# Performance work log

Hardware: AMD Instinct MI355X
Metric: run time of the kernel (lower is better)

The kernel has to match this reference:

```python
import jax, jax.numpy as jnp
import numpy as np
import math

# ----- sizes -----
NUM_EDGES = 16384
NUM_NODES = 1024          # senders index into [0, NUM_NODES)
N_MUL = 64                # multiplicity n = V.shape[1]
AVG_NEIGH = 16.0          # avg_num_neighbors
F_IN = 64                 # scalar feature dim of x

# ----- real spherical harmonics (component normalization: sum_m Y_lm^2 = 2l+1) -----
_S3 = math.sqrt(3.0); _S5 = math.sqrt(5.0); _S15 = math.sqrt(15.0)
_C33 = math.sqrt(70.0)/4.0; _C32 = math.sqrt(105.0)/2.0
_C31 = math.sqrt(42.0)/4.0; _C30 = math.sqrt(7.0)/2.0; _CXYZ = math.sqrt(105.0)

def _sph(vn):
    x, y, z = vn[:, 0], vn[:, 1], vn[:, 2]
    Y0 = jnp.ones_like(x)[:, None]
    Y1 = _S3 * vn
    Y2 = jnp.stack([_S15*x*y, _S15*y*z, 0.5*_S5*(3*z*z - 1), _S15*x*z, 0.5*_S15*(x*x - y*y)], axis=1)
    Y3 = jnp.stack([_C33*y*(3*x*x - y*y), _CXYZ*x*y*z, _C31*y*(5*z*z - 1), _C30*z*(5*z*z - 3), _C31*x*(5*z*z - 1), _C32*z*(x*x - y*y), _C33*x*(x*x - 3*y*y)], axis=1)
    return [Y0, Y1, Y2, Y3]

# monomial form of the same SH, used to derive EXACT Clebsch-Gordan coefficients
_SHP = {
    0: [[(1.0, (0,0,0))]],
    1: [[(_S3, (1,0,0))], [(_S3, (0,1,0))], [(_S3, (0,0,1))]],
    2: [[(_S15, (1,1,0))], [(_S15, (0,1,1))], [(1.5*_S5, (0,0,2)), (-0.5*_S5, (0,0,0))], [(_S15, (1,0,1))], [(0.5*_S15, (2,0,0)), (-0.5*_S15, (0,2,0))]],
    3: [[(3*_C33, (2,1,0)), (-_C33, (0,3,0))], [(_CXYZ, (1,1,1))], [(5*_C31, (0,1,2)), (-_C31, (0,1,0))], [(5*_C30, (0,0,3)), (-3*_C30, (0,0,1))], [(5*_C31, (1,0,2)), (-_C31, (1,0,0))], [(_C32, (2,0,1)), (-_C32, (0,2,1))], [(_C33, (3,0,0)), (-3*_C33, (1,2,0))]],
}

def _dfact(n):
    r = 1
    while n > 1:
        r *= n; n -= 2
    return r

def _mono_int(e):
    # exact integral of x^a y^b z^c over the unit sphere
    a, b, c = e
    if (a % 2) or (b % 2) or (c % 2):
        return 0.0
    return 4.0*math.pi*_dfact(a-1)*_dfact(b-1)*_dfact(c-1)/_dfact(a+b+c+1)

def _pmul(p, q):
    return [(cp*cq, (a1+a2, b1+b2, c1+c2)) for cp, (a1,b1,c1) in p for cq, (a2,b2,c2) in q]

def _pint(p):
    return sum(c*_mono_int(e) for c, e in p)

def _cg(l1, l2, l3):
    # unique SO(3) intertwiner in this real-SH basis, scaled like e3nn component norm: sqrt(2l3+1)*w3j
    C = np.zeros((2*l1+1, 2*l2+1, 2*l3+1))
    for i, p1 in enumerate(_SHP[l1]):
        for j, p2 in enumerate(_SHP[l2]):
            p12 = _pmul(p1, p2)
            for k, p3 in enumerate(_SHP[l3]):
                C[i, j, k] = _pint(_pmul(p12, p3)) / (4.0*math.pi)
    return jnp.asarray(C / np.linalg.norm(C) * np.sqrt(2*l3+1), dtype=jnp.float32)

# tensor-product paths surviving filter_ir_out = 0e + 1o + 2e (inputs: SH 0e+1o+2e+3o, V 0e+1o+2e)
_PATHS0 = [(0,0), (1,1), (2,2)]
_PATHS1 = [(0,1), (1,0), (1,2), (2,1), (3,2)]
_PATHS2 = [(0,2), (1,1), (2,0), (2,2), (3,1)]
CGS = {(l1, l2, l3): _cg(l1, l2, l3) for l3, ps in ((0, _PATHS0), (1, _PATHS1), (2, _PATHS2)) for l1, l2 in ps}

# e3nn normalize_function(silu): divide by sqrt(E_{z~N(0,1)}[silu(z)^2])
_zg = np.linspace(-12.0, 12.0, 200001)
_phi = np.exp(-0.5*_zg*_zg)/np.sqrt(2.0*np.pi)
_sl = _zg/(1.0 + np.exp(-_zg))
ACT_C = float(np.sqrt(np.sum(_sl*_sl*_phi)*(_zg[1]-_zg[0])))

def _nsilu(v):
    return jax.nn.silu(v) / ACT_C

def _forward(vectors, x, V, senders, W_w, W1, W2, W3, Wv1, Wv2):
    E, n = V.shape[0], V.shape[1]
    d = jnp.linalg.norm(vectors, axis=1, keepdims=True)                 # [E,1] edge lengths
    vn = vectors / d
    Y = jnp.concatenate(_sph(vn), axis=1)                               # [E,16], ell = 0..3
    w = (x @ W_w) / math.sqrt(x.shape[1])                               # [E,n] edge weights (1-layer MLP, no act)
    wY = w[:, :, None] * Y[:, None, :]                                  # [E,n,16]
    agg = jax.ops.segment_sum(wY, senders, num_segments=NUM_NODES)[senders]  # scatter_sum + map_back
    agg = agg / math.sqrt(AVG_NEIGH)
    A = jnp.split(agg, [1, 4, 9], axis=2)                               # SH chunks: dims 1,3,5,7
    B = jnp.split(V, [1, 4], axis=2)                                    # V chunks: dims 1,3,5
    def tp(l1, l2, l3):
        return jnp.einsum('eni,enj,ijk->enk', A[l1], B[l2], CGS[(l1, l2, l3)])
    scal = jnp.concatenate([tp(a, b, 0) for a, b in _PATHS0], axis=2)   # [E,n,3] new scalars
    V1 = jnp.concatenate([tp(a, b, 1) for a, b in _PATHS1], axis=1)     # [E,5n,3] 1o paths
    V2 = jnp.concatenate([tp(a, b, 2) for a, b in _PATHS2], axis=1)     # [E,5n,5] 2e paths
    h = jnp.concatenate([x, scal.reshape(E, 3*n)], axis=1)              # [E, F_IN+3n]
    h = _nsilu(h @ W1 / math.sqrt(h.shape[1]))
    h = _nsilu(h @ W2 / math.sqrt(W2.shape[0]))
    h = h @ W3 / math.sqrt(W3.shape[0])                                 # output_activation=False
    # poly_envelope(p-1=5, 2), p=6: 1 - 28 d^6 + 48 d^7 - 21 d^8 on [0,1), 0 outside
    u = 1.0 - 28.0*d**6 + 48.0*d**7 - 21.0*d**8
    x_out = jnp.where(d < 1.0, u, 0.0) * h                              # [E,64]
    o1 = jnp.einsum('emi,mo->eoi', V1, Wv1) / math.sqrt(V1.shape[1])    # Linear per irrep: [E,n,3]
    o2 = jnp.einsum('emi,mo->eoi', V2, Wv2) / math.sqrt(V2.shape[1])    # [E,n,5]
    # output 0e block has no input path -> zeros (e3nn Linear, no bias)
    V_out = jnp.concatenate([jnp.zeros((E, n, 1), x_out.dtype), o1, o2], axis=2)  # [E,n,9]
    return x_out, V_out

def setup_inputs():
    key = jax.random.key(0)
    ks = jax.random.split(key, 10)
    E = NUM_EDGES
    vectors = 0.35 * jax.random.normal(ks[0], (E, 3), jnp.float32)   # mostly inside cutoff radius 1
    x = jax.random.normal(ks[1], (E, F_IN), jnp.float32)
    V = jax.random.normal(ks[2], (E, N_MUL, 9), jnp.float32)
    senders = jax.random.randint(ks[3], (E,), 0, NUM_NODES, dtype=jnp.int32)
    W_w = jax.random.normal(ks[4], (F_IN, N_MUL), jnp.float32)
    W1 = jax.random.normal(ks[5], (F_IN + 3*N_MUL, 64), jnp.float32)
    W2 = jax.random.normal(ks[6], (64, 64), jnp.float32)
    W3 = jax.random.normal(ks[7], (64, 64), jnp.float32)
    Wv1 = jax.random.normal(ks[8], (5*N_MUL, N_MUL), jnp.float32)
    Wv2 = jax.random.normal(ks[9], (5*N_MUL, N_MUL), jnp.float32)
    return {"vectors": vectors, "x": x, "V": V, "senders": senders, "W_w": W_w, "W1": W1, "W2": W2, "W3": W3, "Wv1": Wv1, "Wv2": Wv2}

def reference(vectors, x, V, senders, W_w, W1, W2, W3, Wv1, Wv2):
    return _forward(vectors, x, V, senders, W_w, W1, W2, W3, Wv1, Wv2)
```

## Files before the change

### kernel.cpp

```cpp
#include <hip/hip_runtime.h>
#include <math.h>

#define NNODES 1024
#define EB 4

typedef __attribute__((ext_vector_type(8))) short short8;
typedef __attribute__((ext_vector_type(4))) float f32x4;

__device__ __forceinline__ unsigned short f2bf(float f) {
  union { float f; unsigned int u; } v; v.f = f;
  unsigned int r = v.u + 0x7fffu + ((v.u >> 16) & 1u);
  return (unsigned short)(r >> 16);
}

__device__ __constant__ int PL1[13] = {0,1,2, 0,1,1,2,3, 0,1,2,2,3};
__device__ __constant__ int PL2[13] = {0,1,2, 1,0,2,1,2, 2,1,0,2,1};
__device__ __constant__ int PL3[13] = {0,0,0, 1,1,1,1,1, 2,2,2,2,2};
__device__ __constant__ int PCG[13] = {0,1,10, 35,44,53,98,143, 248,273,318,343,468};

__device__ __constant__ double SHC[16][2] = {
  {1.0, 0.0},
  {1.7320508075688772, 0.0},
  {1.7320508075688772, 0.0},
  {1.7320508075688772, 0.0},
  {3.8729833462074170, 0.0},
  {3.8729833462074170, 0.0},
  {3.3541019662496844, -1.1180339887498949},
  {3.8729833462074170, 0.0},
  {1.9364916731037085, -1.9364916731037085},
  {6.2749501990055667, -2.0916500663351889},
  {10.246950765959598, 0.0},
  {8.1009258730098255, -1.6201851746019651},
  {6.6143782776614768, -3.9686269665968861},
  {8.1009258730098255, -1.6201851746019651},
  {5.1234753829797990, -5.1234753829797990},
  {2.0916500663351889, -6.2749501990055667},
};
__device__ __constant__ int SHE[16][2] = {
  {0,0},{1,0},{16,0},{256,0},
  {17,0},{272,0},{512,0},{257,0},{2,32},
  {18,48},{273,0},{528,16},{768,256},{513,1},{258,288},{3,33}};

__global__ __launch_bounds__(256) void k_const(
    float* __restrict__ cg, float* __restrict__ actp, int* __restrict__ counts)
{
  const int bid = blockIdx.x;
  const int t = threadIdx.x;

  if (bid < 13) {
    if (bid < 4) counts[bid*256 + t] = 0;
    __shared__ double sh[256];
    const int p = bid;
    const int LOFF[4] = {0,1,4,9};
    int l1 = PL1[p], l2 = PL2[p], l3 = PL3[p];
    int n1 = 2*l1+1, n2 = 2*l2+1, n3 = 2*l3+1;
    int nent = n1*n2*n3;
    const unsigned long long DP =
        1ULL | (1ULL<<7) | (1ULL<<14) | (2ULL<<21) | (3ULL<<28)
      | (8ULL<<35) | (15ULL<<42) | (48ULL<<49) | (105ULL<<56);
    double v = 0.0;
    if (t < nent) {
      int i = t / (n2*n3);
      int rem = t - i*(n2*n3);
      int j = rem / n3;
      int k = rem - j*n3;
      int lm1 = LOFF[l1]+i, lm2 = LOFF[l2]+j, lm3 = LOFF[l3]+k;
      double cs1[2] = {SHC[lm1][0], SHC[lm1][1]}; int es1[2] = {SHE[lm1][0], SHE[lm1][1]};
      double cs2[2] = {SHC[lm2][0], SHC[lm2][1]}; int es2[2] = {SHE[lm2][0], SHE[lm2][1]};
      double cs3[2] = {SHC[lm3][0], SHC[lm3][1]}; int es3[2] = {SHE[lm3][0], SHE[lm3][1]};
      #pragma unroll
      for (int t1 = 0; t1 < 2; t1++)
      #pragma unroll
      for (int t2 = 0; t2 < 2; t2++)
      #pragma unroll
      for (int t3 = 0; t3 < 2; t3++) {
        double cc = cs1[t1]*cs2[t2]*cs3[t3];
        int s = es1[t1] + es2[t2] + es3[t3];
        int a = s & 15, b = (s >> 4) & 15, c = (s >> 8) & 15;
        if (!((a|b|c) & 1)) {
          double num = (double)(int)((DP >> (7*a)) & 127)
                     * (double)(int)((DP >> (7*b)) & 127)
                     * (double)(int)((DP >> (7*c)) & 127);
          double den = (double)(int)((DP >> (7*(a+b+c+2))) & 127);
          v += cc * (num / den);
        }
      }
    }
    sh[t] = (t < nent) ? v*v : 0.0;
    __syncthreads();
    for (int d = 128; d > 0; d >>= 1) {
      if (t < d) sh[t] += sh[t+d];
      __syncthreads();
    }
    double scale = sqrt((double)(2*l3+1)) / sqrt(sh[0]);
    if (t < nent) cg[PCG[p] + t] = (float)(v * scale * 0.25);

  } else {
    __shared__ float shf[256];
    const int b = bid - 13;
    const float dz = 24.0f / 200000.0f;
    float s = 0.f;
    for (int i = b*256 + t; i <= 200000; i += 8*256) {
      float z = -12.0f + dz * (float)i;
      float ph = __expf(-0.5f * z * z) * 0.3989422804014327f;
      float sl = z / (1.f + __expf(-z));
      s = fmaf(sl*sl, ph, s);
    }
    shf[t] = s;
    __syncthreads();
    for (int d = 128; d > 0; d >>= 1) {
      if (t < d) shf[t] += shf[t + d];
      __syncthreads();
    }
    if (t == 0) actp[b] = shf[0];
  }
}

__global__ __launch_bounds__(256) void k_pre(
    const int* __restrict__ senders, int* __restrict__ counts, int* __restrict__ elist,
    const float* __restrict__ Wv1, const float* __restrict__ Wv2,
    const float* __restrict__ W1, const float* __restrict__ W2, const float* __restrict__ W3,
    unsigned short* __restrict__ wv1f, unsigned short* __restrict__ wv2f,
    unsigned short* __restrict__ w1f, unsigned short* __restrict__ w2f,
    unsigned short* __restrict__ w3f,
    const float* __restrict__ actp, int E)
{
  const int t = threadIdx.x;
  const int nsc = gridDim.x - 32;
  if ((int)blockIdx.x < nsc) {
    int e = blockIdx.x*256 + t;
    if (e < E) {
      int s = senders[e];
      int pos = atomicAdd(&counts[s], 1) & 63;
      elist[s*64 + pos] = e;
    }
    return;
  }
  const int wid = t >> 6, lane = t & 63;
  const int g = (blockIdx.x - nsc)*4 + wid;
  const float ia = rsqrtf((actp[0]+actp[1]+actp[2]+actp[3]
                          +actp[4]+actp[5]+actp[6]+actp[7]) * (24.0f/200000.0f));
  const float s320 = 0.05590169943749474f;
  const float* src; unsigned short* dst; int nk, f; float sc;
  if (g < 40)       { src = Wv1; dst = wv1f; nk = 10; f = g;       sc = s320; }
  else if (g < 80)  { src = Wv2; dst = wv2f; nk = 10; f = g - 40;  sc = s320; }
  else if (g < 112) { src = W1;  dst = w1f;  nk = 8;  f = g - 80;  sc = 0.0625f; }
  else if (g < 120) { src = W2;  dst = w2f;  nk = 2;  f = g - 112; sc = 0.125f*ia; }
  else              { src = W3;  dst = w3f;  nk = 2;  f = g - 120; sc = 0.125f*ia; }
  int nt = f / nk;
  int ks = f - nt*nk;
  unsigned short us[8];
  #pragma unroll
  for (int j = 0; j < 8; j++) {
    float v = src[(ks*32 + (lane>>4)*8 + j)*64 + nt*16 + (lane & 15)];
    us[j] = f2bf(v * sc);
  }
  uint4 pk;
  pk.x = (unsigned)us[0] | ((unsigned)us[1] << 16);
  pk.y = (unsigned)us[2] | ((unsigned)us[3] << 16);
  pk.z = (unsigned)us[4] | ((unsigned)us[5] << 16);
  pk.w = (unsigned)us[6] | ((unsigned)us[7] << 16);
  *(uint4*)(dst + ((size_t)f*64 + lane)*8) = pk;
}

__global__ __launch_bounds__(256) void k_node(
    const float* __restrict__ vec, const float* __restrict__ x,
    const float* __restrict__ Ww,
    const int* __restrict__ counts, const int* __restrict__ elist,
    float* __restrict__ node_agg)
{
  __shared__ float red[4*1024];
  const int wid = threadIdx.x >> 6, lane = threadIdx.x & 63;
  const int s = blockIdx.x;
  const int deg = min(counts[s], 64);

  const float S3 = 1.7320508075688772f, S5 = 2.23606797749979f, S15 = 3.872983346207417f;
  const float C33 = 2.091650066335189f, C32 = 5.123475382979799f, C31 = 1.6201851746019651f;
  const float C30 = 1.3228756555322954f, CX = 10.246950765959598f;

  float A[16];
  #pragma unroll
  for (int k = 0; k < 16; k++) A[k] = 0.f;

  for (int ii = wid; ii < deg; ii += 4) {
    int e = elist[s*64 + ii];
    float xv = x[(size_t)e*64 + lane];
    float w = 0.f;
    #pragma unroll
    for (int f = 0; f < 64; f++)
      w = fmaf(__shfl(xv, f), Ww[f*64 + lane], w);
    w *= 0.125f;
    float vx = vec[e*3+0], vy = vec[e*3+1], vz = vec[e*3+2];
    float d = sqrtf(vx*vx + vy*vy + vz*vz);
    float X = vx/d, Yv = vy/d, Z = vz/d;
    float y[16];
    y[0] = 1.f;
    y[1] = S3*X;  y[2] = S3*Yv;  y[3] = S3*Z;
    y[4] = S15*X*Yv; y[5] = S15*Yv*Z; y[6] = 0.5f*S5*(3.f*Z*Z - 1.f);
    y[7] = S15*X*Z;  y[8] = 0.5f*S15*(X*X - Yv*Yv);
    y[9]  = C33*Yv*(3.f*X*X - Yv*Yv);
    y[10] = CX*X*Yv*Z;
    y[11] = C31*Yv*(5.f*Z*Z - 1.f);
    y[12] = C30*Z*(5.f*Z*Z - 3.f);
    y[13] = C31*X*(5.f*Z*Z - 1.f);
    y[14] = C32*Z*(X*X - Yv*Yv);
    y[15] = C33*X*(X*X - 3.f*Yv*Yv);
    #pragma unroll
    for (int k = 0; k < 16; k++) A[k] = fmaf(w, y[k], A[k]);
  }
  #pragma unroll
  for (int k = 0; k < 16; k++) red[wid*1024 + lane*16 + k] = A[k];
  __syncthreads();
  const int t = threadIdx.x;
  f32x4 v0 = ((f32x4*)red)[t];
  f32x4 v1 = ((f32x4*)red)[256 + t];
  f32x4 v2 = ((f32x4*)red)[512 + t];
  f32x4 v3 = ((f32x4*)red)[768 + t];
  f32x4 sum = v0 + v1 + v2 + v3;
  ((f32x4*)(node_agg + (size_t)s*1024))[t] = sum;
}

template<int L1, int L2, int L3>
__device__ __forceinline__ void tp_path(const float* __restrict__ cgp,
    const float a[16], const float b[9], float o[2*L3+1])
{
  constexpr int N1 = 2*L1+1, N2 = 2*L2+1, N3 = 2*L3+1;
  constexpr int AO = (L1==0) ? 0 : (L1==1) ? 1 : (L1==2) ? 4 : 9;
  constexpr int BO = (L2==0) ? 0 : (L2==1) ? 1 : 4;
  constexpr int LM1 = (L1==0) ? 0 : (L1==1) ? 1 : (L1==2) ? 4 : 9;
  constexpr int LM2 = (L2==0) ? 0 : (L2==1) ? 1 : 4;
  constexpr int LM3 = (L3==0) ? 0 : (L3==1) ? 1 : 4;
  static constexpr unsigned char PAR[16] =
      {0, 1,2,4, 3,6,0,5,0, 2,7,2,4,1,4,1};
  #pragma unroll
  for (int k = 0; k < N3; k++) o[k] = 0.f;
  int ci = 0;
  #pragma unroll
  for (int i = 0; i < N1; i++) {
    #pragma unroll
    for (int j = 0; j < N2; j++) {
      float ab = a[AO+i] * b[BO+j];
      #pragma unroll
      for (int k = 0; k < N3; k++) {
        if ((PAR[LM1+i] ^ PAR[LM2+j] ^ PAR[LM3+k]) == 0)
          o[k] = fmaf(ab, cgp[ci], o[k]);
        ci++;
      }
    }
  }
}

__global__ __launch_bounds__(256, 6) void edge_main(
    const float* __restrict__ vec, const float* __restrict__ x,
    const float* __restrict__ V, const int* __restrict__ senders,
    const float* __restrict__ node_agg, const float* __restrict__ cg,
    const unsigned short* __restrict__ wv1f, const unsigned short* __restrict__ wv2f,
    const unsigned short* __restrict__ w1f, const unsigned short* __restrict__ w2f,
    const unsigned short* __restrict__ w3f,
    float* __restrict__ out, int E)
{
  __shared__ __align__(16) unsigned short V12sh[32*328];
  __shared__ __align__(16) unsigned short zrow[336];
  __shared__ __align__(16) unsigned short hsh[4*264];
  __shared__ __align__(16) unsigned short h1sh[4*72];
  __shared__ __align__(16) unsigned short h2sh[4*72];
  __shared__ float ush[EB];

  unsigned short* V1sh = V12sh;
  unsigned short* V2sh = V12sh + 12*328;
  float* vosh = (float*)V12sh;

  const int t = threadIdx.x;
  const int wid = t >> 6, lane = t & 63;
  const int e0 = blockIdx.x * EB;
  const size_t E64 = (size_t)E * 64;

  if (t < 168) ((unsigned int*)zrow)[t] = 0u;

  if (t < 64) {
    int el = t >> 4, off = (t & 15)*4;
    f32x4 xv = *(const f32x4*)(x + (size_t)(e0 + el)*64 + off);
    uint2 pk;
    pk.x = (unsigned)f2bf(xv.x) | ((unsigned)f2bf(xv.y) << 16);
    pk.y = (unsigned)f2bf(xv.z) | ((unsigned)f2bf(xv.w) << 16);
    *(uint2*)(hsh + el*264 + off) = pk;
  }

  {
    const int eloc = wid;
    const int eg = e0 + eloc;

    float b[9];
    const float* vp = V + (size_t)eg*576 + lane*9;
    #pragma unroll
    for (int j = 0; j < 9; j++) b[j] = vp[j];

    const int s = senders[eg];
    float a[16];
    const float* nap = node_agg + s*1024 + lane*16;
    #pragma unroll
    for (int k = 0; k < 16; k++) a[k] = nap[k];

    float o1[1], o3[3], o5[5];
    tp_path<0,0,0>(cg + 0,  a, b, o1); hsh[eloc*264 + 64 + lane*3 + 0] = f2bf(o1[0]);
    tp_path<1,1,0>(cg + 1,  a, b, o1); hsh[eloc*264 + 64 + lane*3 + 1] = f2bf(o1[0]);
    tp_path<2,2,0>(cg + 10, a, b, o1); hsh[eloc*264 + 64 + lane*3 + 2] = f2bf(o1[0]);
    tp_path<0,1,1>(cg + 35, a, b, o3);
    { int r = eloc*3; for (int i=0;i<3;i++) V1sh[(r+i)*328 + 0*64 + lane] = f2bf(o3[i]); }
    tp_path<1,0,1>(cg + 44, a, b, o3);
    { int r = eloc*3; for (int i=0;i<3;i++) V1sh[(r+i)*328 + 1*64 + lane] = f2bf(o3[i]); }
    tp_path<1,2,1>(cg + 53, a, b, o3);
    { int r = eloc*3; for (int i=0;i<3;i++) V1sh[(r+i)*328 + 2*64 + lane] = f2bf(o3[i]); }
    tp_path<2,1,1>(cg + 98, a, b, o3);
    { int r = eloc*3; for (int i=0;i<3;i++) V1sh[(r+i)*328 + 3*64 + lane] = f2bf(o3[i]); }
    tp_path<3,2,1>(cg + 143, a, b, o3);
    { int r = eloc*3; for (int i=0;i<3;i++) V1sh[(r+i)*328 + 4*64 + lane] = f2bf(o3[i]); }
    tp_path<0,2,2>(cg + 248, a, b, o5);
    { int r = eloc*5; for (int i=0;i<5;i++) V2sh[(r+i)*328 + 0*64 + lane] = f2bf(o5[i]); }
    tp_path<1,1,2>(cg + 273, a, b, o5);
    { int r = eloc*5; for (int i=0;i<5;i++) V2sh[(r+i)*328 + 1*64 + lane] = f2bf(o5[i]); }
    tp_path<2,0,2>(cg + 318, a, b, o5);
    { int r = eloc*5; for (int i=0;i<5;i++) V2sh[(r+i)*328 + 2*64 + lane] = f2bf(o5[i]); }
    tp_path<2,2,2>(cg + 343, a, b, o5);
    { int r = eloc*5; for (int i=0;i<5;i++) V2sh[(r+i)*328 + 3*64 + lane] = f2bf(o5[i]); }
    tp_path<3,1,2>(cg + 468, a, b, o5);
    { int r = eloc*5; for (int i=0;i<5;i++) V2sh[(r+i)*328 + 4*64 + lane] = f2bf(o5[i]); }

    if (lane == 0) {
      float vx = vec[eg*3+0], vy = vec[eg*3+1], vz = vec[eg*3+2];
      float d = sqrtf(vx*vx + vy*vy + vz*vz);
      float u = 0.f;
      if (d < 1.f) {
        float d3 = d*d*d, d6 = d3*d3, d7 = d6*d, d8 = d7*d;
        u = 1.f - 28.f*d6 + 48.f*d7 - 21.f*d8;
      }
      ush[eloc] = u;
    }
  }
  __syncthreads();

  const int ntile = wid;
  const int qr = lane >> 4;
  const int ml = lane & 15;

  f32x4 acc1 = (f32x4){0,0,0,0};
  {
    const unsigned short* p0 = (ml < 12) ? &V1sh[ml*328] : zrow;
    const unsigned short* bb = wv1f + ((size_t)(ntile*10)*64 + lane)*8;
    #pragma unroll
    for (int ks = 0; ks < 10; ks++) {
      short8 bf = *(const short8*)(bb + ks*512);
      short8 af = *(const short8*)(p0 + ks*32 + qr*8);
      acc1 = __builtin_amdgcn_mfma_f32_16x16x32_bf16(af, bf, acc1, 0, 0, 0);
    }
  }

  f32x4 acc2a = (f32x4){0,0,0,0}, acc2b = (f32x4){0,0,0,0};
  {
    const unsigned short* p0 = &V2sh[ml*328];
    const unsigned short* p1 = (16+ml < 20) ? &V2sh[(16+ml)*328] : zrow;
    const unsigned short* bb = wv2f + ((size_t)(ntile*10)*64 + lane)*8;
    #pragma unroll
    for (int ks = 0; ks < 10; ks++) {
      short8 bf = *(const short8*)(bb + ks*512);
      int ao = ks*32 + qr*8;
      short8 af0 = *(const short8*)(p0 + ao);
      short8 af1 = *(const short8*)(p1 + ao);
      acc2a = __builtin_amdgcn_mfma_f32_16x16x32_bf16(af0, bf, acc2a, 0, 0, 0);
      acc2b = __builtin_amdgcn_mfma_f32_16x16x32_bf16(af1, bf, acc2b, 0, 0, 0);
    }
  }

  const unsigned short* hp = (ml < 4) ? &hsh[ml*264] : zrow;
  {
    f32x4 c = (f32x4){0,0,0,0};
    const unsigned short* bb = w1f + ((size_t)(ntile*8)*64 + lane)*8;
    #pragma unroll
    for (int ks = 0; ks < 8; ks++) {
      short8 bf = *(const short8*)(bb + ks*512);
      short8 af = *(const short8*)(hp + ks*32 + qr*8);
      c = __builtin_amdgcn_mfma_f32_16x16x32_bf16(af, bf, c, 0, 0, 0);
    }
    #pragma unroll
    for (int r = 0; r < 4; r++) {
      int row = qr*4 + r;
      if (row < 4) {
        float v = c[r];
        float sv = v / (1.f + expf(-v));
        h1sh[row*72 + ntile*16 + ml] = f2bf(sv);
      }
    }
  }
  __syncthreads();

  #pragma unroll
  for (int r = 0; r < 4; r++) {
    int row = qr*4 + r;
    if (row < 12) {
      int el = row / 3, i = row - (row/3)*3;
      vosh[el*584 + (ntile*16+ml)*9 + 1 + i] = acc1[r];
    }
  }
  #pragma unroll
  for (int r = 0; r < 4; r++) {
    int row = qr*4 + r;
    int el = row / 5, i = row - (row/5)*5;
    vosh[el*584 + (ntile*16+ml)*9 + 4 + i] = acc2a[r];
  }
  #pragma unroll
  for (int r = 0; r < 4; r++) {
    int row = 16 + qr*4 + r;
    if (row < 20) {
      int el = row / 5, i = row - (row/5)*5;
      vosh[el*584 + (ntile*16+ml)*9 + 4 + i] = acc2b[r];
    }
  }
  { int el = t >> 6, o = t & 63;
    vosh[el*584 + o*9] = 0.f; }

  {
    f32x4 c = (f32x4){0,0,0,0};
    const unsigned short* ap = (ml < 4) ? &h1sh[ml*72] : zrow;
    const unsigned short* bb = w2f + ((size_t)(ntile*2)*64 + lane)*8;
    #pragma unroll
    for (int ks = 0; ks < 2; ks++) {
      short8 bf = *(const short8*)(bb + ks*512);
      short8 af = *(const short8*)(ap + ks*32 + qr*8);
      c = __builtin_amdgcn_mfma_f32_16x16x32_bf16(af, bf, c, 0, 0, 0);
    }
    #pragma unroll
    for (int r = 0; r < 4; r++) {
      int row = qr*4 + r;
      if (row < 4) {
        float v = c[r];
        float sv = v / (1.f + expf(-v));
        h2sh[row*72 + ntile*16 + ml] = f2bf(sv);
      }
    }
  }
  __syncthreads();

  {
    f32x4 c = (f32x4){0,0,0,0};
    const unsigned short* ap = (ml < 4) ? &h2sh[ml*72] : zrow;
    const unsigned short* bb = w3f + ((size_t)(ntile*2)*64 + lane)*8;
    #pragma unroll
    for (int ks = 0; ks < 2; ks++) {
      short8 bf = *(const short8*)(bb + ks*512);
      short8 af = *(const short8*)(ap + ks*32 + qr*8);
      c = __builtin_amdgcn_mfma_f32_16x16x32_bf16(af, bf, c, 0, 0, 0);
    }
    #pragma unroll
    for (int r = 0; r < 4; r++) {
      int row = qr*4 + r;
      if (row < 4) {
        out[(size_t)(e0+row)*64 + ntile*16 + ml] = ush[row] * c[r];
      }
    }
  }

  for (int q = t; q < 576; q += 256) {
    int el = q / 144, i4 = q - (q/144)*144;
    ((f32x4*)(out + E64 + (size_t)(e0+el)*576))[i4] = ((f32x4*)(vosh + el*584))[i4];
  }
}

extern "C" void kernel_launch(void* const* d_in, const int* in_sizes, int n_in,
                              void* d_out, int out_size, void* d_ws, size_t ws_size,
                              hipStream_t stream)
{
  const float* vec     = (const float*)d_in[0];
  const float* x       = (const float*)d_in[1];
  const float* V       = (const float*)d_in[2];
  const int*   senders = (const int*)  d_in[3];
  const float* Ww      = (const float*)d_in[4];
  const float* W1      = (const float*)d_in[5];
  const float* W2      = (const float*)d_in[6];
  const float* W3      = (const float*)d_in[7];
  const float* Wv1     = (const float*)d_in[8];
  const float* Wv2     = (const float*)d_in[9];
  float* out = (float*)d_out;
  const int E = in_sizes[0] / 3;

  char* base = (char*)d_ws;
  float* node_agg = (float*)(base);
  float* cgbuf    = (float*)(base + (8<<20));
  float* actp     = (float*)(base + (8<<20) + 4096);
  int* counts     = (int*)  (base + (8<<20) + 8192);
  int* elist      = (int*)  (base + (8<<20) + 12288);
  unsigned short* wv1f = (unsigned short*)(base + (8<<20) + 278528);
  unsigned short* wv2f = (unsigned short*)(base + (8<<20) + 319488);
  unsigned short* w1f  = (unsigned short*)(base + (8<<20) + 360448);
  unsigned short* w2f  = (unsigned short*)(base + (8<<20) + 393216);
  unsigned short* w3f  = (unsigned short*)(base + (8<<20) + 401408);

  const int nsc = (E + 255) >> 8;
  k_const<<<21, 256, 0, stream>>>(cgbuf, actp, counts);
  k_pre<<<nsc + 32, 256, 0, stream>>>(senders, counts, elist,
                                      Wv1, Wv2, W1, W2, W3,
                                      wv1f, wv2f, w1f, w2f, w3f, actp, E);
  k_node<<<NNODES, 256, 0, stream>>>(vec, x, Ww, counts, elist, node_agg);
  edge_main<<<E/EB, 256, 0, stream>>>(vec, x, V, senders, node_agg, cgbuf,
                                      wv1f, wv2f, w1f, w2f, w3f, out, E);
}
```

Baseline: 178.0 us.

## Precompute CG and activation constants on host, batch 8 edges per block

Drops the k_const kernel: Clebsch-Gordan coefficients and the activation normalization constant are computed once on the host in a static object, passed as a kernel argument struct, and counts are zeroed with a memset. edge_main now processes 8 edges per block, which gives fuller MFMA tiles and staged, coalesced output writes, but uses more shared memory and lowers the occupancy hint. k_node caches the Ww column in registers and splits the dot product across four accumulators. The host-side constants depend only on fixed math, not on inputs, so this is legitimate precomputation.

After: 171.8 us. 3.5% less time.

```diff
diff --git a/kernel.cpp b/kernel.cpp
--- a/kernel.cpp
+++ b/kernel.cpp
@@ -2,7 +2,7 @@
 #include <math.h>
 
 #define NNODES 1024
-#define EB 4
+#define EB 8
 
 typedef __attribute__((ext_vector_type(8))) short short8;
 typedef __attribute__((ext_vector_type(4))) float f32x4;
@@ -13,12 +13,9 @@
   return (unsigned short)(r >> 16);
 }
 
-__device__ __constant__ int PL1[13] = {0,1,2, 0,1,1,2,3, 0,1,2,2,3};
-__device__ __constant__ int PL2[13] = {0,1,2, 1,0,2,1,2, 2,1,0,2,1};
-__device__ __constant__ int PL3[13] = {0,0,0, 1,1,1,1,1, 2,2,2,2,2};
-__device__ __constant__ int PCG[13] = {0,1,10, 35,44,53,98,143, 248,273,318,343,468};
-
-__device__ __constant__ double SHC[16][2] = {
+struct CGPack { float v[576]; };
+
+static const double H_SHC[16][2] = {
   {1.0, 0.0},
   {1.7320508075688772, 0.0},
   {1.7320508075688772, 0.0},
@@ -36,85 +33,59 @@
   {5.1234753829797990, -5.1234753829797990},
   {2.0916500663351889, -6.2749501990055667},
 };
-__device__ __constant__ int SHE[16][2] = {
+static const int H_SHE[16][2] = {
   {0,0},{1,0},{16,0},{256,0},
   {17,0},{272,0},{512,0},{257,0},{2,32},
   {18,48},{273,0},{528,16},{768,256},{513,1},{258,288},{3,33}};
-
-__global__ __launch_bounds__(256) void k_const(
-    float* __restrict__ cg, float* __restrict__ actp, int* __restrict__ counts)
-{
-  const int bid = blockIdx.x;
-  const int t = threadIdx.x;
-
-  if (bid < 13) {
-    if (bid < 4) counts[bid*256 + t] = 0;
-    __shared__ double sh[256];
-    const int p = bid;
+static const int H_PL1[13] = {0,1,2, 0,1,1,2,3, 0,1,2,2,3};
+static const int H_PL2[13] = {0,1,2, 1,0,2,1,2, 2,1,0,2,1};
+static const int H_PL3[13] = {0,0,0, 1,1,1,1,1, 2,2,2,2,2};
+static const int H_PCG[13] = {0,1,10, 35,44,53,98,143, 248,273,318,343,468};
+
+static double h_dfact(int n) { double r = 1.0; while (n > 1) { r *= n; n -= 2; } return r; }
+
+struct HostConsts {
+  CGPack pack;
+  float inv_actc;
+  HostConsts() {
     const int LOFF[4] = {0,1,4,9};
-    int l1 = PL1[p], l2 = PL2[p], l3 = PL3[p];
-    int n1 = 2*l1+1, n2 = 2*l2+1, n3 = 2*l3+1;
-    int nent = n1*n2*n3;
-    const unsigned long long DP =
-        1ULL | (1ULL<<7) | (1ULL<<14) | (2ULL<<21) | (3ULL<<28)
-      | (8ULL<<35) | (15ULL<<42) | (48ULL<<49) | (105ULL<<56);
-    double v = 0.0;
-    if (t < nent) {
-      int i = t / (n2*n3);
-      int rem = t - i*(n2*n3);
-      int j = rem / n3;
-      int k = rem - j*n3;
-      int lm1 = LOFF[l1]+i, lm2 = LOFF[l2]+j, lm3 = LOFF[l3]+k;
-      double cs1[2] = {SHC[lm1][0], SHC[lm1][1]}; int es1[2] = {SHE[lm1][0], SHE[lm1][1]};
-      double cs2[2] = {SHC[lm2][0], SHC[lm2][1]}; int es2[2] = {SHE[lm2][0], SHE[lm2][1]};
-      double cs3[2] = {SHC[lm3][0], SHC[lm3][1]}; int es3[2] = {SHE[lm3][0], SHE[lm3][1]};
-      #pragma unroll
-      for (int t1 = 0; t1 < 2; t1++)
-      #pragma unroll
-      for (int t2 = 0; t2 < 2; t2++)
-      #pragma unroll
-      for (int t3 = 0; t3 < 2; t3++) {
-        double cc = cs1[t1]*cs2[t2]*cs3[t3];
-        int s = es1[t1] + es2[t2] + es3[t3];
-        int a = s & 15, b = (s >> 4) & 15, c = (s >> 8) & 15;
-        if (!((a|b|c) & 1)) {
-          double num = (double)(int)((DP >> (7*a)) & 127)
-                     * (double)(int)((DP >> (7*b)) & 127)
-                     * (double)(int)((DP >> (7*c)) & 127);
-          double den = (double)(int)((DP >> (7*(a+b+c+2))) & 127);
-          v += cc * (num / den);
+    for (int p = 0; p < 13; p++) {
+      int l1 = H_PL1[p], l2 = H_PL2[p], l3 = H_PL3[p];
+      int n1 = 2*l1+1, n2 = 2*l2+1, n3 = 2*l3+1, nent = n1*n2*n3;
+      double vals[125], ss = 0.0;
+      for (int t = 0; t < nent; t++) {
+        int i = t / (n2*n3);
+        int rem = t - i*(n2*n3);
+        int j = rem / n3;
+        int k = rem - j*n3;
+        int lm1 = LOFF[l1]+i, lm2 = LOFF[l2]+j, lm3 = LOFF[l3]+k;
+        double v = 0.0;
+        for (int t1 = 0; t1 < 2; t1++)
+        for (int t2 = 0; t2 < 2; t2++)
+        for (int t3 = 0; t3 < 2; t3++) {
+          double cc = H_SHC[lm1][t1]*H_SHC[lm2][t2]*H_SHC[lm3][t3];
+          if (cc == 0.0) continue;
+          int s = H_SHE[lm1][t1] + H_SHE[lm2][t2] + H_SHE[lm3][t3];
+          int a = s & 15, b = (s >> 4) & 15, c = (s >> 8) & 15;
+          if (!((a|b|c) & 1))
+            v += cc * (h_dfact(a-1)*h_dfact(b-1)*h_dfact(c-1) / h_dfact(a+b+c+1));
         }
+        vals[t] = v; ss += v*v;
       }
-    }
-    sh[t] = (t < nent) ? v*v : 0.0;
-    __syncthreads();
-    for (int d = 128; d > 0; d >>= 1) {
-      if (t < d) sh[t] += sh[t+d];
-      __syncthreads();
-    }
-    double scale = sqrt((double)(2*l3+1)) / sqrt(sh[0]);
-    if (t < nent) cg[PCG[p] + t] = (float)(v * scale * 0.25);
-
-  } else {
-    __shared__ float shf[256];
-    const int b = bid - 13;
-    const float dz = 24.0f / 200000.0f;
-    float s = 0.f;
-    for (int i = b*256 + t; i <= 200000; i += 8*256) {
-      float z = -12.0f + dz * (float)i;
-      float ph = __expf(-0.5f * z * z) * 0.3989422804014327f;
-      float sl = z / (1.f + __expf(-z));
-      s = fmaf(sl*sl, ph, s);
-    }
-    shf[t] = s;
-    __syncthreads();
-    for (int d = 128; d > 0; d >>= 1) {
-      if (t < d) shf[t] += shf[t + d];
-      __syncthreads();
-    }
-    if (t == 0) actp[b] = shf[0];
-  }
-}
+      double scale = sqrt((double)(2*l3+1)) / sqrt(ss);
+      for (int t = 0; t < nent; t++) pack.v[H_PCG[p]+t] = (float)(vals[t]*scale*0.25);
+    }
+    pack.v[573] = pack.v[574] = pack.v[575] = 0.f;
+    double s = 0.0, dz = 24.0/200000.0;
+    for (int i = 0; i <= 200000; i++) {
+      double z = -12.0 + dz*i;
+      double ph = exp(-0.5*z*z) * 0.39894228040143267794;
+      double sl = z / (1.0 + exp(-z));
+      s += sl*sl*ph;
+    }
+    inv_actc = (float)(1.0 / sqrt(s*dz));
+  }
+};
 
 __global__ __launch_bounds__(256) void k_pre(
     const int* __restrict__ senders, int* __restrict__ counts, int* __restrict__ elist,
@@ -123,7 +94,7 @@
     unsigned short* __restrict__ wv1f, unsigned short* __restrict__ wv2f,
     unsigned short* __restrict__ w1f, unsigned short* __restrict__ w2f,
     unsigned short* __restrict__ w3f,
-    const float* __restrict__ actp, int E)
+    float inv_actc, int E)
 {
   const int t = threadIdx.x;
   const int nsc = gridDim.x - 32;
@@ -138,8 +109,7 @@
   }
   const int wid = t >> 6, lane = t & 63;
   const int g = (blockIdx.x - nsc)*4 + wid;
-  const float ia = rsqrtf((actp[0]+actp[1]+actp[2]+actp[3]
-                          +actp[4]+actp[5]+actp[6]+actp[7]) * (24.0f/200000.0f));
+  const float ia = inv_actc;
   const float s320 = 0.05590169943749474f;
   const float* src; unsigned short* dst; int nk, f; float sc;
   if (g < 40)       { src = Wv1; dst = wv1f; nk = 10; f = g;       sc = s320; }
@@ -163,7 +133,7 @@
   *(uint4*)(dst + ((size_t)f*64 + lane)*8) = pk;
 }
 
-__global__ __launch_bounds__(256) void k_node(
+__global__ __launch_bounds__(256, 2) void k_node(
     const float* __restrict__ vec, const float* __restrict__ x,
     const float* __restrict__ Ww,
     const int* __restrict__ counts, const int* __restrict__ elist,
@@ -174,6 +144,10 @@
   const int s = blockIdx.x;
   const int deg = min(counts[s], 64);
 
+  float ww[64];
+  #pragma unroll
+  for (int f = 0; f < 64; f++) ww[f] = Ww[f*64 + lane];
+
   const float S3 = 1.7320508075688772f, S5 = 2.23606797749979f, S15 = 3.872983346207417f;
   const float C33 = 2.091650066335189f, C32 = 5.123475382979799f, C31 = 1.6201851746019651f;
   const float C30 = 1.3228756555322954f, CX = 10.246950765959598f;
@@ -185,11 +159,15 @@
   for (int ii = wid; ii < deg; ii += 4) {
     int e = elist[s*64 + ii];
     float xv = x[(size_t)e*64 + lane];
-    float w = 0.f;
-    #pragma unroll
-    for (int f = 0; f < 64; f++)
-      w = fmaf(__shfl(xv, f), Ww[f*64 + lane], w);
-    w *= 0.125f;
+    float w0 = 0.f, w1 = 0.f, w2 = 0.f, w3 = 0.f;
+    #pragma unroll
+    for (int f = 0; f < 64; f += 4) {
+      w0 = fmaf(__shfl(xv, f+0), ww[f+0], w0);
+      w1 = fmaf(__shfl(xv, f+1), ww[f+1], w1);
+      w2 = fmaf(__shfl(xv, f+2), ww[f+2], w2);
+      w3 = fmaf(__shfl(xv, f+3), ww[f+3], w3);
+    }
+    float w = ((w0+w1)+(w2+w3)) * 0.125f;
     float vx = vec[e*3+0], vy = vec[e*3+1], vz = vec[e*3+2];
     float d = sqrtf(vx*vx + vy*vy + vz*vz);
     float X = vx/d, Yv = vy/d, Z = vz/d;
@@ -250,25 +228,28 @@
   }
 }
 
-__global__ __launch_bounds__(256, 6) void edge_main(
+__global__ __launch_bounds__(256, 3) void edge_main(
     const float* __restrict__ vec, const float* __restrict__ x,
     const float* __restrict__ V, const int* __restrict__ senders,
-    const float* __restrict__ node_agg, const float* __restrict__ cg,
+    const float* __restrict__ node_agg, const CGPack P,
     const unsigned short* __restrict__ wv1f, const unsigned short* __restrict__ wv2f,
     const unsigned short* __restrict__ w1f, const unsigned short* __restrict__ w2f,
     const unsigned short* __restrict__ w3f,
     float* __restrict__ out, int E)
 {
-  __shared__ __align__(16) unsigned short V12sh[32*328];
+  __shared__ __align__(16) unsigned short V12sh[64*328];
   __shared__ __align__(16) unsigned short zrow[336];
-  __shared__ __align__(16) unsigned short hsh[4*264];
-  __shared__ __align__(16) unsigned short h1sh[4*72];
-  __shared__ __align__(16) unsigned short h2sh[4*72];
+  __shared__ __align__(16) unsigned short hsh[8*264];
+  __shared__ __align__(16) unsigned short h1sh[8*72];
+  __shared__ __align__(16) unsigned short h2sh[8*72];
+  __shared__ __align__(16) float xosh[8*64];
   __shared__ float ush[EB];
 
   unsigned short* V1sh = V12sh;
-  unsigned short* V2sh = V12sh + 12*328;
+  unsigned short* V2sh = V12sh + 24*328;
   float* vosh = (float*)V12sh;
+
+  const float* cg = P.v;
 
   const int t = threadIdx.x;
   const int wid = t >> 6, lane = t & 63;
@@ -277,7 +258,7 @@
 
   if (t < 168) ((unsigned int*)zrow)[t] = 0u;
 
-  if (t < 64) {
+  if (t < 128) {
     int el = t >> 4, off = (t & 15)*4;
     f32x4 xv = *(const f32x4*)(x + (size_t)(e0 + el)*64 + off);
     uint2 pk;
@@ -286,8 +267,9 @@
     *(uint2*)(hsh + el*264 + off) = pk;
   }
 
-  {
-    const int eloc = wid;
+  #pragma unroll
+  for (int sub = 0; sub < 2; sub++) {
+    const int eloc = wid*2 + sub;
     const int eg = e0 + eloc;
 
     float b[9];
@@ -343,37 +325,44 @@
   const int qr = lane >> 4;
   const int ml = lane & 15;
 
-  f32x4 acc1 = (f32x4){0,0,0,0};
+  f32x4 acc1a = (f32x4){0,0,0,0}, acc1b = (f32x4){0,0,0,0};
   {
-    const unsigned short* p0 = (ml < 12) ? &V1sh[ml*328] : zrow;
+    const unsigned short* p0 = &V1sh[ml*328];
+    const unsigned short* p1 = (16+ml < 24) ? &V1sh[(16+ml)*328] : zrow;
     const unsigned short* bb = wv1f + ((size_t)(ntile*10)*64 + lane)*8;
-    #pragma unroll
-    for (int ks = 0; ks < 10; ks++) {
-      short8 bf = *(const short8*)(bb + ks*512);
-      short8 af = *(const short8*)(p0 + ks*32 + qr*8);
-      acc1 = __builtin_amdgcn_mfma_f32_16x16x32_bf16(af, bf, acc1, 0, 0, 0);
-    }
-  }
-
-  f32x4 acc2a = (f32x4){0,0,0,0}, acc2b = (f32x4){0,0,0,0};
-  {
-    const unsigned short* p0 = &V2sh[ml*328];
-    const unsigned short* p1 = (16+ml < 20) ? &V2sh[(16+ml)*328] : zrow;
-    const unsigned short* bb = wv2f + ((size_t)(ntile*10)*64 + lane)*8;
     #pragma unroll
     for (int ks = 0; ks < 10; ks++) {
       short8 bf = *(const short8*)(bb + ks*512);
       int ao = ks*32 + qr*8;
       short8 af0 = *(const short8*)(p0 + ao);
       short8 af1 = *(const short8*)(p1 + ao);
+      acc1a = __builtin_amdgcn_mfma_f32_16x16x32_bf16(af0, bf, acc1a, 0, 0, 0);
+      acc1b = __builtin_amdgcn_mfma_f32_16x16x32_bf16(af1, bf, acc1b, 0, 0, 0);
+    }
+  }
+
+  f32x4 acc2a = (f32x4){0,0,0,0}, acc2b = (f32x4){0,0,0,0}, acc2c = (f32x4){0,0,0,0};
+  {
+    const unsigned short* p0 = &V2sh[ml*328];
+    const unsigned short* p1 = &V2sh[(16+ml)*328];
+    const unsigned short* p2 = (32+ml < 40) ? &V2sh[(32+ml)*328] : zrow;
+    const unsigned short* bb = wv2f + ((size_t)(ntile*10)*64 + lane)*8;
+    #pragma unroll
+    for (int ks = 0; ks < 10; ks++) {
+      short8 bf = *(const short8*)(bb + ks*512);
+      int ao = ks*32 + qr*8;
+      short8 af0 = *(const short8*)(p0 + ao);
+      short8 af1 = *(const short8*)(p1 + ao);
+      short8 af2 = *(const short8*)(p2 + ao);
       acc2a = __builtin_amdgcn_mfma_f32_16x16x32_bf16(af0, bf, acc2a, 0, 0, 0);
       acc2b = __builtin_amdgcn_mfma_f32_16x16x32_bf16(af1, bf, acc2b, 0, 0, 0);
-    }
-  }
-
-  const unsigned short* hp = (ml < 4) ? &hsh[ml*264] : zrow;
+      acc2c = __builtin_amdgcn_mfma_f32_16x16x32_bf16(af2, bf, acc2c, 0, 0, 0);
+    }
+  }
+
   {
     f32x4 c = (f32x4){0,0,0,0};
+    const unsigned short* hp = (ml < 8) ? &hsh[ml*264] : zrow;
     const unsigned short* bb = w1f + ((size_t)(ntile*8)*64 + lane)*8;
     #pragma unroll
     for (int ks = 0; ks < 8; ks++) {
@@ -384,7 +373,7 @@
     #pragma unroll
     for (int r = 0; r < 4; r++) {
       int row = qr*4 + r;
-      if (row < 4) {
+      if (row < 8) {
         float v = c[r];
         float sv = v / (1.f + expf(-v));
         h1sh[row*72 + ntile*16 + ml] = f2bf(sv);
@@ -396,9 +385,15 @@
   #pragma unroll
   for (int r = 0; r < 4; r++) {
     int row = qr*4 + r;
-    if (row < 12) {
+    int el = row / 3, i = row - (row/3)*3;
+    vosh[el*584 + (ntile*16+ml)*9 + 1 + i] = acc1a[r];
+  }
+  #pragma unroll
+  for (int r = 0; r < 4; r++) {
+    int row = 16 + qr*4 + r;
+    if (row < 24) {
       int el = row / 3, i = row - (row/3)*3;
-      vosh[el*584 + (ntile*16+ml)*9 + 1 + i] = acc1[r];
+      vosh[el*584 + (ntile*16+ml)*9 + 1 + i] = acc1b[r];
     }
   }
   #pragma unroll
@@ -410,17 +405,25 @@
   #pragma unroll
   for (int r = 0; r < 4; r++) {
     int row = 16 + qr*4 + r;
-    if (row < 20) {
+    int el = row / 5, i = row - (row/5)*5;
+    vosh[el*584 + (ntile*16+ml)*9 + 4 + i] = acc2b[r];
+  }
+  #pragma unroll
+  for (int r = 0; r < 4; r++) {
+    int row = 32 + qr*4 + r;
+    if (row < 40) {
       int el = row / 5, i = row - (row/5)*5;
-      vosh[el*584 + (ntile*16+ml)*9 + 4 + i] = acc2b[r];
-    }
-  }
-  { int el = t >> 6, o = t & 63;
-    vosh[el*584 + o*9] = 0.f; }
+      vosh[el*584 + (ntile*16+ml)*9 + 4 + i] = acc2c[r];
+    }
+  }
+  for (int q = t; q < 8*64; q += 256) {
+    int el = q >> 6, n = q & 63;
+    vosh[el*584 + n*9] = 0.f;
+  }
 
   {
     f32x4 c = (f32x4){0,0,0,0};
-    const unsigned short* ap = (ml < 4) ? &h1sh[ml*72] : zrow;
+    const unsigned short* ap = (ml < 8) ? &h1sh[ml*72] : zrow;
     const unsigned short* bb = w2f + ((size_t)(ntile*2)*64 + lane)*8;
     #pragma unroll
     for (int ks = 0; ks < 2; ks++) {
@@ -431,7 +434,7 @@
     #pragma unroll
     for (int r = 0; r < 4; r++) {
       int row = qr*4 + r;
-      if (row < 4) {
+      if (row < 8) {
         float v = c[r];
         float sv = v / (1.f + expf(-v));
         h2sh[row*72 + ntile*16 + ml] = f2bf(sv);
@@ -442,7 +445,7 @@
 
   {
     f32x4 c = (f32x4){0,0,0,0};
-    const unsigned short* ap = (ml < 4) ? &h2sh[ml*72] : zrow;
+    const unsigned short* ap = (ml < 8) ? &h2sh[ml*72] : zrow;
     const unsigned short* bb = w3f + ((size_t)(ntile*2)*64 + lane)*8;
     #pragma unroll
     for (int ks = 0; ks < 2; ks++) {
@@ -453,16 +456,18 @@
     #pragma unroll
     for (int r = 0; r < 4; r++) {
       int row = qr*4 + r;
-      if (row < 4) {
-        out[(size_t)(e0+row)*64 + ntile*16 + ml] = ush[row] * c[r];
-      }
-    }
-  }
-
-  for (int q = t; q < 576; q += 256) {
+      if (row < 8) xosh[row*64 + ntile*16 + ml] = ush[row] * c[r];
+    }
+  }
+
+  for (int q = t; q < 8*144; q += 256) {
     int el = q / 144, i4 = q - (q/144)*144;
     ((f32x4*)(out + E64 + (size_t)(e0+el)*576))[i4] = ((f32x4*)(vosh + el*584))[i4];
   }
+  __syncthreads();
+
+  if (t < 128)
+    ((f32x4*)(out + (size_t)e0*64))[t] = ((f32x4*)xosh)[t];
 }
 
 extern "C" void kernel_launch(void* const* d_in, const int* in_sizes, int n_in,
@@ -482,10 +487,10 @@
   float* out = (float*)d_out;
   const int E = in_sizes[0] / 3;
 
+  static HostConsts HC;
+
   char* base = (char*)d_ws;
   float* node_agg = (float*)(base);
-  float* cgbuf    = (float*)(base + (8<<20));
-  float* actp     = (float*)(base + (8<<20) + 4096);
   int* counts     = (int*)  (base + (8<<20) + 8192);
   int* elist      = (int*)  (base + (8<<20) + 12288);
   unsigned short* wv1f = (unsigned short*)(base + (8<<20) + 278528);
@@ -494,12 +499,13 @@
   unsigned short* w2f  = (unsigned short*)(base + (8<<20) + 393216);
   unsigned short* w3f  = (unsigned short*)(base + (8<<20) + 401408);
 
+  hipMemsetAsync(counts, 0, NNODES*sizeof(int), stream);
+
   const int nsc = (E + 255) >> 8;
-  k_const<<<21, 256, 0, stream>>>(cgbuf, actp, counts);
   k_pre<<<nsc + 32, 256, 0, stream>>>(senders, counts, elist,
                                       Wv1, Wv2, W1, W2, W3,
-                                      wv1f, wv2f, w1f, w2f, w3f, actp, E);
+                                      wv1f, wv2f, w1f, w2f, w3f, HC.inv_actc, E);
   k_node<<<NNODES, 256, 0, stream>>>(vec, x, Ww, counts, elist, node_agg);
-  edge_main<<<E/EB, 256, 0, stream>>>(vec, x, V, senders, node_agg, cgbuf,
+  edge_main<<<E/EB, 256, 0, stream>>>(vec, x, V, senders, node_agg, HC.pack,
                                       wv1f, wv2f, w1f, w2f, w3f, out, E);
 }
```
